# Performance work log

Hardware: AMD Instinct MI355X
Metric: run time of the kernel (lower is better)

## Reference

```python
import jax, jax.numpy as jnp
import numpy as np

N_NODES = 100000
N_EDGES = 1600000
D_IN = 256
D_HID = 128
N_CLASSES = 64
NEG_SLOPE = 0.2


def setup_inputs() -> dict:
    key = jax.random.key(0)
    ks = jax.random.split(key, 8)
    node_features = jax.random.normal(ks[0], (N_NODES, D_IN), dtype=jnp.float32)
    W = jax.random.normal(ks[1], (D_IN, D_HID), dtype=jnp.float32) * (1.0 / np.sqrt(D_IN))
    attn_l = jax.random.normal(ks[2], (D_HID,), dtype=jnp.float32) * (1.0 / np.sqrt(D_HID))
    attn_r = jax.random.normal(ks[3], (D_HID,), dtype=jnp.float32) * (1.0 / np.sqrt(D_HID))
    fc_W = jax.random.normal(ks[4], (D_HID, N_CLASSES), dtype=jnp.float32) * (1.0 / np.sqrt(D_HID))
    fc_b = jnp.zeros((N_CLASSES,), dtype=jnp.float32)
    src = jax.random.randint(ks[5], (N_EDGES,), 0, N_NODES, dtype=jnp.int32)
    dst = jax.random.randint(ks[6], (N_EDGES,), 0, N_NODES, dtype=jnp.int32)
    return dict(node_features=node_features, W=W, attn_l=attn_l, attn_r=attn_r,
                fc_W=fc_W, fc_b=fc_b, src=src, dst=dst)


def reference(node_features, W, attn_l, attn_r, fc_W, fc_b, src, dst):
    N = node_features.shape[0]
    # GATConv (single head): linear projection
    feat = node_features @ W                       # [N, H]
    el = feat @ attn_l                             # [N]
    er = feat @ attn_r                             # [N]
    e = jax.nn.leaky_relu(el[src] + er[dst], NEG_SLOPE)  # [E]
    # segment softmax over incoming edges of each destination node
    m = jax.ops.segment_max(e, dst, num_segments=N)      # [N]
    ex = jnp.exp(e - m[dst])                              # [E]
    denom = jax.ops.segment_sum(ex, dst, num_segments=N)  # [N]
    a = ex / denom[dst]                                   # [E]
    # attention-weighted neighbor aggregation (scatter-add)
    msg = a[:, None] * feat[src]                           # [E, H]
    h = jax.ops.segment_sum(msg, dst, num_segments=N)     # [N, H]
    # num_heads=1 -> h.mean(1) over heads is identity; final Linear
    return h @ fc_W + fc_b                                 # [N, C]
```

## Files before the change

### kernel.cpp

```cpp
#include <hip/hip_runtime.h>
#include <math.h>

#define NN 100000
#define NE 1600000
#define DIN 256
#define DHID 128
#define NCLS 64
#define NEG_SLOPE 0.2f

#define NBUCK 196
#define ECAP 10240
#define CHUNK 4096
#define NCHB ((NE + CHUNK - 1) / CHUNK)
#define PREPB 16

#define NGRP 16384
#define G1 ((NN + 127) / 128)

typedef __bf16 bf16_t;
typedef bf16_t bf16x8 __attribute__((ext_vector_type(8)));
typedef float f32x4 __attribute__((ext_vector_type(4)));
typedef ushort ushort8v __attribute__((ext_vector_type(8)));

__device__ __forceinline__ ushort f2bf(float f) {
    union { float f; unsigned u; } c; c.f = f;
    unsigned u = c.u;
    unsigned r = (u + 0x7FFFu + ((u >> 16) & 1u)) >> 16;
    return (ushort)r;
}
__device__ __forceinline__ float bf2f(ushort b) {
    return __uint_as_float(((unsigned)b) << 16);
}

__global__ __launch_bounds__(256) void k_prep(const float* __restrict__ W,
                                              const float* __restrict__ fcW,
                                              ushort* __restrict__ Wt,
                                              ushort* __restrict__ fcWt,
                                              int* __restrict__ gcur) {
    int t = blockIdx.x * 256 + threadIdx.x;
    if (blockIdx.x == 0) gcur[threadIdx.x] = 0;
    for (int i = t; i < DHID * DIN; i += PREPB * 256) {
        int n = i >> 8, k = i & 255;
        Wt[i] = f2bf(W[k * DHID + n]);
    }
    for (int i = t; i < NCLS * DHID; i += PREPB * 256) {
        int n = i >> 7, k = i & 127;
        fcWt[i] = f2bf(fcW[k * NCLS + n]);
    }
}

union SmemB {
    struct {
        int hist[NBUCK];
        int scn[256];
        int loff[NBUCK];
        int cur[NBUCK];
        int gb[NBUCK];
        unsigned ord[CHUNK];
        ushort obk[CHUNK];
    } b;
    struct {
        ushort Xs[2][8192];
        ushort Wl[2][8192];
        float Al[DHID];
        float Ar[DHID];
    } g;
};

#define ISSUE(XA, WA, KC) do { \
    int k0g_ = (KC) * 64; \
    _Pragma("unroll") \
    for (int i_ = 0; i_ < 4; i_++) { \
        int grow_ = row0 + srow[i_]; \
        if (grow_ < NN) { \
            const float4* p_ = (const float4*)(X + (size_t)grow_ * DIN + k0g_ + ske[i_]); \
            XA[i_][0] = p_[0]; XA[i_][1] = p_[1]; \
        } else { \
            XA[i_][0] = make_float4(0.f,0.f,0.f,0.f); \
            XA[i_][1] = make_float4(0.f,0.f,0.f,0.f); \
        } \
        WA[i_] = *(const uint4*)(Wt + (size_t)srow[i_] * DIN + k0g_ + ske[i_]); \
    } \
} while (0)

#define COMMIT(XA, WA, BUF) do { \
    _Pragma("unroll") \
    for (int i_ = 0; i_ < 4; i_++) { \
        int o_ = i_ * 4096 + t * 16; \
        ushort8v bb_; \
        bb_[0] = f2bf(XA[i_][0].x); bb_[1] = f2bf(XA[i_][0].y); \
        bb_[2] = f2bf(XA[i_][0].z); bb_[3] = f2bf(XA[i_][0].w); \
        bb_[4] = f2bf(XA[i_][1].x); bb_[5] = f2bf(XA[i_][1].y); \
        bb_[6] = f2bf(XA[i_][1].z); bb_[7] = f2bf(XA[i_][1].w); \
        *(ushort8v*)((char*)&sm.g.Xs[BUF][0] + o_) = bb_; \
        *(uint4*)((char*)&sm.g.Wl[BUF][0] + o_) = WA[i_]; \
    } \
} while (0)

#define COMPUTE(BUF) do { \
    const char* xb_ = (const char*)&sm.g.Xs[BUF][0]; \
    const char* wb_ = (const char*)&sm.g.Wl[BUF][0]; \
    _Pragma("unroll") \
    for (int k0_ = 0; k0_ < 2; k0_++) { \
        int kb_ = k0_ * 64 + kgrp; \
        bf16x8 a_[2], b_[8]; \
        _Pragma("unroll") \
        for (int r_ = 0; r_ < 2; r_++) { \
            int row_ = rbase + r_ * 16 + lcol; \
            a_[r_] = *(const bf16x8*)(xb_ + row_ * 128 + (kb_ ^ ((row_ & 7) << 4))); \
        } \
        _Pragma("unroll") \
        for (int cc_ = 0; cc_ < 8; cc_++) { \
            int n_ = cc_ * 16 + lcol; \
            b_[cc_] = *(const bf16x8*)(wb_ + n_ * 128 + (kb_ ^ ((n_ & 7) << 4))); \
        } \
        _Pragma("unroll") \
        for (int r_ = 0; r_ < 2; r_++) \
            _Pragma("unroll") \
            for (int cc_ = 0; cc_ < 8; cc_++) \
                acc[r_][cc_] = __builtin_amdgcn_mfma_f32_16x16x32_bf16(a_[r_], b_[cc_], acc[r_][cc_], 0, 0, 0); \
    } \
} while (0)

__global__ __launch_bounds__(256, 2) void fused_bin_gemm1(
        const int* __restrict__ src, const int* __restrict__ dst,
        int* __restrict__ gcur, unsigned* __restrict__ ebuf,
        const float* __restrict__ X, const ushort* __restrict__ Wt,
        const float* __restrict__ attn_l, const float* __restrict__ attn_r,
        ushort* __restrict__ featb, float* __restrict__ el, float* __restrict__ er) {
    __shared__ SmemB sm;
    const int t = threadIdx.x;

    if (blockIdx.x < NCHB) {
        const int base = blockIdx.x * CHUNK;
        int cnt = NE - base; if (cnt > CHUNK) cnt = CHUNK;

        for (int i = t; i < NBUCK; i += 256) sm.b.hist[i] = 0;
        __syncthreads();

        unsigned vals[16];
        int bks[16];
#pragma unroll
        for (int i = 0; i < 16; i++) {
            int idx = base + i * 256 + t;
            if (idx < NE) {
                int d = dst[idx], s = src[idx];
                int bb = d >> 9;
                bks[i] = bb;
                vals[i] = ((unsigned)(d & 511) << 17) | (unsigned)s;
                atomicAdd(&sm.b.hist[bb], 1);
            } else bks[i] = -1;
        }
        __syncthreads();

        int hv = (t < NBUCK) ? sm.b.hist[t] : 0;
        sm.b.scn[t] = hv;
        __syncthreads();
        for (int d = 1; d < 256; d <<= 1) {
            int a = (t >= d) ? sm.b.scn[t - d] : 0;
            __syncthreads();
            sm.b.scn[t] += a;
            __syncthreads();
        }
        if (t < NBUCK) { sm.b.loff[t] = sm.b.scn[t] - hv; sm.b.cur[t] = sm.b.scn[t] - hv; }
        __syncthreads();

#pragma unroll
        for (int i = 0; i < 16; i++) {
            if (bks[i] >= 0) {
                int slot = atomicAdd(&sm.b.cur[bks[i]], 1);
                sm.b.ord[slot] = vals[i];
                sm.b.obk[slot] = (ushort)bks[i];
            }
        }
        if (t < NBUCK && hv > 0) sm.b.gb[t] = t * ECAP + atomicAdd(&gcur[t], hv);
        __syncthreads();

        for (int s = t; s < cnt; s += 256) {
            int bb = sm.b.obk[s];
            ebuf[sm.b.gb[bb] + (s - sm.b.loff[bb])] = sm.b.ord[s];
        }
        return;
    }

    const int row0 = (blockIdx.x - NCHB) * 128;
    if (t < 128) { sm.g.Al[t] = attn_l[t]; sm.g.Ar[t] = attn_r[t]; }

    int srow[4], ske[4];
#pragma unroll
    for (int i = 0; i < 4; i++) {
        int o = i * 4096 + t * 16;
        int row = o >> 7;
        int bl = (o & 127) ^ ((row & 7) << 4);
        srow[i] = row;
        ske[i] = bl >> 1;
    }

    const int w = t >> 6, lane = t & 63;
    const int rbase = w * 32;
    const int lcol = lane & 15;
    const int kgrp = (lane >> 4) * 16;

    f32x4 acc[2][8];
#pragma unroll
    for (int r = 0; r < 2; r++)
#pragma unroll
        for (int c = 0; c < 8; c++) acc[r][c] = (f32x4){0.f, 0.f, 0.f, 0.f};

    float4 xA[4][2], xB[4][2];
    uint4  wA[4], wB[4];

    ISSUE(xA, wA, 0); COMMIT(xA, wA, 0);
    ISSUE(xB, wB, 1);
    __syncthreads();
    ISSUE(xA, wA, 2); COMPUTE(0); COMMIT(xB, wB, 1); __syncthreads();
    ISSUE(xB, wB, 3); COMPUTE(1); COMMIT(xA, wA, 0); __syncthreads();
    COMPUTE(0); COMMIT(xB, wB, 1); __syncthreads();
    COMPUTE(1);

    __syncthreads();
    ushort* Os = (ushort*)sm.g.Xs;
#pragma unroll
    for (int r = 0; r < 2; r++)
#pragma unroll
        for (int cc = 0; cc < 8; cc++)
#pragma unroll
            for (int i = 0; i < 4; i++) {
                int rloc = rbase + r * 16 + (lane >> 4) * 4 + i;
                int col = cc * 16 + lcol;
                Os[rloc * 128 + col] = f2bf(acc[r][cc][i]);
            }
    __syncthreads();

    {
        int row = t >> 1, half = t & 1;
        int grow = row0 + row;
        const ushort* orow = Os + row * 128 + half * 64;
        const float* alp = sm.g.Al + half * 64;
        const float* arp = sm.g.Ar + half * 64;
        float pl = 0.f, pr = 0.f;
        int rot = row & 7;
#pragma unroll
        for (int qq = 0; qq < 8; qq++) {
            int q = (qq + rot) & 7;
            ushort8v f8 = *(const ushort8v*)(orow + q * 8);
#pragma unroll
            for (int e = 0; e < 8; e++) {
                float fe = bf2f(f8[e]);
                pl += fe * alp[q * 8 + e];
                pr += fe * arp[q * 8 + e];
            }
        }
        pl += __shfl_down(pl, 1);
        pr += __shfl_down(pr, 1);
        if (!half && grow < NN) { el[grow] = pl; er[grow] = pr; }
    }

#pragma unroll
    for (int i = 0; i < 8; i++) {
        int u = i * 256 + t;
        int row = u >> 4;
        int grow = row0 + row;
        if (grow < NN)
            *(uint4*)(featb + (size_t)grow * 128 + (u & 15) * 8) =
                *(uint4*)((char*)Os + u * 16);
    }
}

__global__ __launch_bounds__(1024) void fused_csr(const unsigned* __restrict__ ebuf,
                                                  const int* __restrict__ gcur,
                                                  int* __restrict__ off_g,
                                                  int* __restrict__ deg_g,
                                                  int* __restrict__ ssrc,
                                                  int* __restrict__ nsplit) {
    __shared__ int sdeg[512];
    __shared__ int pr[256];
    __shared__ int lofs[512];
    __shared__ int scnt[512];
    __shared__ int sb[2];
    const int b = blockIdx.x, t = threadIdx.x;
    const int node0 = b << 9;
    const int ebase = b * ECAP;
    const int ecnt = gcur[b];

    if (t < 256) pr[t] = (t < NBUCK) ? gcur[t] : 0;
    __syncthreads();
    for (int d = 1; d < 256; d <<= 1) {
        int a = 0;
        if (t < 256 && t >= d) a = pr[t - d];
        __syncthreads();
        if (t < 256) pr[t] += a;
        __syncthreads();
    }
    if (t == 0) { sb[0] = pr[b] - ecnt; sb[1] = pr[NBUCK - 1]; }
    if (t < 512) sdeg[t] = 0;
    __syncthreads();

    for (int s = t; s < ecnt; s += 1024)
        atomicAdd(&sdeg[ebuf[ebase + s] >> 17], 1);
    __syncthreads();

    int d0 = 0, d1 = 0;
    if (t < 256) { d0 = sdeg[2 * t]; d1 = sdeg[2 * t + 1]; pr[t] = d0 + d1; }
    __syncthreads();
    for (int d = 1; d < 256; d <<= 1) {
        int a = 0;
        if (t < 256 && t >= d) a = pr[t - d];
        __syncthreads();
        if (t < 256) pr[t] += a;
        __syncthreads();
    }
    if (t < 256) {
        int ex = pr[t] - d0 - d1;
        lofs[2 * t] = ex;
        lofs[2 * t + 1] = ex + d0;
        scnt[2 * t] = 0; scnt[2 * t + 1] = 0;
        int n0 = node0 + 2 * t, n1 = n0 + 1;
        if (n0 < NN) { off_g[n0] = ebase + ex;      deg_g[n0] = d0; }
        if (n1 < NN) { off_g[n1] = ebase + ex + d0; deg_g[n1] = d1; }
    }
    __syncthreads();

    for (int s = t; s < ecnt; s += 1024) {
        unsigned v = ebuf[ebase + s];
        int dl = v >> 17;
        int c = atomicAdd(&scnt[dl], 1);
        ssrc[ebase + lofs[dl] + c] = (int)(v & 0x1FFFFu);
    }

    {
        long bpre_b = sb[0], total = sb[1];
        if (total > 0 && ecnt > 0) {
            long glo = (bpre_b * NGRP + total - 1) / total;
            long ghi = ((bpre_b + ecnt) * NGRP + total - 1) / total;
            if (ghi > NGRP) ghi = NGRP;
            for (long g = glo + t; g < ghi; g += 1024) {
                long target = g * total / NGRP;
                int lt = (int)(target - bpre_b);
                int lo = 0, hi = 512;
                while (lo < hi) {
                    int m = (lo + hi) >> 1;
                    if (lofs[m] < lt) lo = m + 1; else hi = m;
                }
                int node = node0 + lo;
                if (node > NN) node = NN;
                nsplit[g] = node;
            }
        }
        if (b == 0 && t == 0) nsplit[NGRP] = NN;
    }
}

__global__ __launch_bounds__(256) void aggregate(const int* __restrict__ off,
                                                 const int* __restrict__ deg,
                                                 const int* __restrict__ ssrc,
                                                 const float* __restrict__ el,
                                                 const float* __restrict__ er,
                                                 const ushort* __restrict__ featb,
                                                 ushort* __restrict__ hb,
                                                 const int* __restrict__ nsplit) {
    const int gid = blockIdx.x * 16 + (threadIdx.x >> 4);
    const int lc = threadIdx.x & 15;
    int n = nsplit[gid];
    const int nend = nsplit[gid + 1];
    const ushort* fb = featb + lc * 8;

    for (; n < nend; ++n) {
        const int e0 = off[n];
        const int dg = deg[n];
        const float erd = er[n];
        float acc[8];
#pragma unroll
        for (int q = 0; q < 8; q++) acc[q] = 0.f;
        float wsum = 0.f;

        int j = 0;
        for (; j + 4 <= dg; j += 4) {
            int s0 = ssrc[e0 + j + 0];
            int s1 = ssrc[e0 + j + 1];
            int s2 = ssrc[e0 + j + 2];
            int s3 = ssrc[e0 + j + 3];
            ushort8v f0 = *(const ushort8v*)(fb + (size_t)s0 * DHID);
            ushort8v f1 = *(const ushort8v*)(fb + (size_t)s1 * DHID);
            ushort8v f2 = *(const ushort8v*)(fb + (size_t)s2 * DHID);
            ushort8v f3 = *(const ushort8v*)(fb + (size_t)s3 * DHID);
            float x0 = el[s0] + erd, x1 = el[s1] + erd;
            float x2 = el[s2] + erd, x3 = el[s3] + erd;
            x0 = x0 > 0.f ? x0 : NEG_SLOPE * x0;
            x1 = x1 > 0.f ? x1 : NEG_SLOPE * x1;
            x2 = x2 > 0.f ? x2 : NEG_SLOPE * x2;
            x3 = x3 > 0.f ? x3 : NEG_SLOPE * x3;
            float w0 = __expf(x0), w1 = __expf(x1);
            float w2 = __expf(x2), w3 = __expf(x3);
            wsum += (w0 + w1) + (w2 + w3);
#pragma unroll
            for (int q = 0; q < 8; q++)
                acc[q] += (w0 * bf2f(f0[q]) + w1 * bf2f(f1[q])) +
                          (w2 * bf2f(f2[q]) + w3 * bf2f(f3[q]));
        }
        for (; j < dg; ++j) {
            int s0 = ssrc[e0 + j];
            ushort8v f0 = *(const ushort8v*)(fb + (size_t)s0 * DHID);
            float x0 = el[s0] + erd;
            x0 = x0 > 0.f ? x0 : NEG_SLOPE * x0;
            float w0 = __expf(x0);
            wsum += w0;
#pragma unroll
            for (int q = 0; q < 8; q++) acc[q] += w0 * bf2f(f0[q]);
        }

        float inv = (dg > 0) ? 1.0f / wsum : 0.f;
        ushort8v o8;
#pragma unroll
        for (int q = 0; q < 8; q++) o8[q] = f2bf(acc[q] * inv);
        *(ushort8v*)(hb + (size_t)n * DHID + lc * 8) = o8;
    }
}

__global__ __launch_bounds__(256, 3) void gemm2(const ushort* __restrict__ hb,
                                                const ushort* __restrict__ fcWt,
                                                const float* __restrict__ fcb,
                                                float* __restrict__ out) {
    __shared__ ushort Hs[128 * 128];
    __shared__ ushort Fs[64 * 128];
    const int t = threadIdx.x;
    const int row0 = blockIdx.x * 128;

    {
#pragma unroll
        for (int i = 0; i < 8; i++) {
            int u = i * 256 + t;
            int row = u >> 4;
            int grow = row0 + row;
            uint4 v = make_uint4(0, 0, 0, 0);
            if (grow < NN) v = *(const uint4*)(hb + (size_t)grow * 128 + (u & 15) * 8);
            int byte_off = row * 256 + (((u & 15) * 16) ^ ((row & 7) << 4));
            *(uint4*)((char*)Hs + byte_off) = v;
        }
#pragma unroll
        for (int i = 0; i < 4; i++) {
            int u = i * 256 + t;
            int n = u >> 4;
            int byte_off = n * 256 + (((u & 15) * 16) ^ ((n & 7) << 4));
            *(uint4*)((char*)Fs + byte_off) = ((const uint4*)fcWt)[u];
        }
    }

    const int w = t >> 6, lane = t & 63;
    const int rbase = w * 32;
    const int lcol = lane & 15;
    const int kgrp = (lane >> 4) * 16;

    f32x4 acc[2][4];
#pragma unroll
    for (int c = 0; c < 4; c++) {
        float bias = fcb[c * 16 + lcol];
#pragma unroll
        for (int r = 0; r < 2; r++)
#pragma unroll
            for (int i = 0; i < 4; i++) acc[r][c][i] = bias;
    }
    __syncthreads();

#pragma unroll
    for (int k0 = 0; k0 < 4; k0++) {
        int kbyte = k0 * 64 + kgrp;
        bf16x8 a[2], b[4];
#pragma unroll
        for (int r = 0; r < 2; r++) {
            int row = rbase + r * 16 + lcol;
            a[r] = *(bf16x8*)((char*)Hs + row * 256 + (kbyte ^ ((row & 7) << 4)));
        }
#pragma unroll
        for (int c = 0; c < 4; c++) {
            int n = c * 16 + lcol;
            b[c] = *(bf16x8*)((char*)Fs + n * 256 + (kbyte ^ ((n & 7) << 4)));
        }
#pragma unroll
        for (int r = 0; r < 2; r++)
#pragma unroll
            for (int c = 0; c < 4; c++)
                acc[r][c] = __builtin_amdgcn_mfma_f32_16x16x32_bf16(a[r], b[c], acc[r][c], 0, 0, 0);
    }

#pragma unroll
    for (int r = 0; r < 2; r++)
#pragma unroll
        for (int i = 0; i < 4; i++) {
            int row = rbase + r * 16 + (lane >> 4) * 4 + i;
            int grow = row0 + row;
            if (grow < NN) {
                float* op = out + (size_t)grow * 64 + lcol;
#pragma unroll
                for (int c = 0; c < 4; c++) op[c * 16] = acc[r][c][i];
            }
        }
}

extern "C" void kernel_launch(void* const* d_in, const int* in_sizes, int n_in,
                              void* d_out, int out_size, void* d_ws, size_t ws_size,
                              hipStream_t stream) {
    const float* X      = (const float*)d_in[0];
    const float* W      = (const float*)d_in[1];
    const float* attn_l = (const float*)d_in[2];
    const float* attn_r = (const float*)d_in[3];
    const float* fcW    = (const float*)d_in[4];
    const float* fcb    = (const float*)d_in[5];
    const int*   src    = (const int*)d_in[6];
    const int*   dst    = (const int*)d_in[7];
    float* out = (float*)d_out;

    char* ws = (char*)d_ws;
    ushort* featb = (ushort*)ws;            ws += (size_t)NN * DHID * 2;
    ushort* hb    = (ushort*)ws;            ws += (size_t)NN * DHID * 2;
    ushort* Wt    = (ushort*)ws;            ws += (size_t)DHID * DIN * 2;
    ushort* fcWt  = (ushort*)ws;            ws += (size_t)NCLS * DHID * 2;
    float* el     = (float*)ws;             ws += (size_t)NN * 4;
    float* er     = (float*)ws;             ws += (size_t)NN * 4;
    int*   deg    = (int*)ws;               ws += (size_t)NN * 4;
    int*   off    = (int*)ws;               ws += (size_t)NN * 4;
    int*   ssrc   = (int*)ws;               ws += (size_t)NBUCK * ECAP * 4;
    unsigned* ebuf = (unsigned*)ws;         ws += (size_t)NBUCK * ECAP * 4;
    int*   gcur   = (int*)ws;               ws += (size_t)256 * 4;
    int*   nsplit = (int*)ws;               ws += (size_t)(NGRP + 1) * 4;

    k_prep<<<PREPB, 256, 0, stream>>>(W, fcW, Wt, fcWt, gcur);
    fused_bin_gemm1<<<NCHB + G1, 256, 0, stream>>>(src, dst, gcur, ebuf,
                                                   X, Wt, attn_l, attn_r, featb, el, er);
    fused_csr<<<NBUCK, 1024, 0, stream>>>(ebuf, gcur, off, deg, ssrc, nsplit);
    aggregate<<<NGRP / 16, 256, 0, stream>>>(off, deg, ssrc, el, er, featb, hb, nsplit);
    gemm2<<<(NN + 127) / 128, 256, 0, stream>>>(hb, fcWt, fcb, out);
}
```

Before: 160.8 us.

## Shrink GEMM1 K-chunk to 32 and raise occupancy to four blocks

Restructures the first-layer projection GEMM to stage 32-wide K slices instead of 64-wide ones, using a loop of eight double-buffered steps with a 64-byte row swizzle. This halves the per-thread prefetch registers and the LDS tile buffers. It also raises launch bounds from 2 to 4 blocks per SM, aiming to hide global-load latency through more resident waves. The trade-off is twice as many block barriers and less MFMA work between them, plus a new swizzle pattern that may bring LDS bank conflicts.

```diff
diff --git a/kernel.cpp b/kernel.cpp
--- a/kernel.cpp
+++ b/kernel.cpp
@@ -60,69 +60,14 @@
         ushort obk[CHUNK];
     } b;
     struct {
-        ushort Xs[2][8192];
-        ushort Wl[2][8192];
+        ushort Xs[2][4096];
+        ushort Wl[2][4096];
         float Al[DHID];
         float Ar[DHID];
     } g;
 };
 
-#define ISSUE(XA, WA, KC) do { \
-    int k0g_ = (KC) * 64; \
-    _Pragma("unroll") \
-    for (int i_ = 0; i_ < 4; i_++) { \
-        int grow_ = row0 + srow[i_]; \
-        if (grow_ < NN) { \
-            const float4* p_ = (const float4*)(X + (size_t)grow_ * DIN + k0g_ + ske[i_]); \
-            XA[i_][0] = p_[0]; XA[i_][1] = p_[1]; \
-        } else { \
-            XA[i_][0] = make_float4(0.f,0.f,0.f,0.f); \
-            XA[i_][1] = make_float4(0.f,0.f,0.f,0.f); \
-        } \
-        WA[i_] = *(const uint4*)(Wt + (size_t)srow[i_] * DIN + k0g_ + ske[i_]); \
-    } \
-} while (0)
-
-#define COMMIT(XA, WA, BUF) do { \
-    _Pragma("unroll") \
-    for (int i_ = 0; i_ < 4; i_++) { \
-        int o_ = i_ * 4096 + t * 16; \
-        ushort8v bb_; \
-        bb_[0] = f2bf(XA[i_][0].x); bb_[1] = f2bf(XA[i_][0].y); \
-        bb_[2] = f2bf(XA[i_][0].z); bb_[3] = f2bf(XA[i_][0].w); \
-        bb_[4] = f2bf(XA[i_][1].x); bb_[5] = f2bf(XA[i_][1].y); \
-        bb_[6] = f2bf(XA[i_][1].z); bb_[7] = f2bf(XA[i_][1].w); \
-        *(ushort8v*)((char*)&sm.g.Xs[BUF][0] + o_) = bb_; \
-        *(uint4*)((char*)&sm.g.Wl[BUF][0] + o_) = WA[i_]; \
-    } \
-} while (0)
-
-#define COMPUTE(BUF) do { \
-    const char* xb_ = (const char*)&sm.g.Xs[BUF][0]; \
-    const char* wb_ = (const char*)&sm.g.Wl[BUF][0]; \
-    _Pragma("unroll") \
-    for (int k0_ = 0; k0_ < 2; k0_++) { \
-        int kb_ = k0_ * 64 + kgrp; \
-        bf16x8 a_[2], b_[8]; \
-        _Pragma("unroll") \
-        for (int r_ = 0; r_ < 2; r_++) { \
-            int row_ = rbase + r_ * 16 + lcol; \
-            a_[r_] = *(const bf16x8*)(xb_ + row_ * 128 + (kb_ ^ ((row_ & 7) << 4))); \
-        } \
-        _Pragma("unroll") \
-        for (int cc_ = 0; cc_ < 8; cc_++) { \
-            int n_ = cc_ * 16 + lcol; \
-            b_[cc_] = *(const bf16x8*)(wb_ + n_ * 128 + (kb_ ^ ((n_ & 7) << 4))); \
-        } \
-        _Pragma("unroll") \
-        for (int r_ = 0; r_ < 2; r_++) \
-            _Pragma("unroll") \
-            for (int cc_ = 0; cc_ < 8; cc_++) \
-                acc[r_][cc_] = __builtin_amdgcn_mfma_f32_16x16x32_bf16(a_[r_], b_[cc_], acc[r_][cc_], 0, 0, 0); \
-    } \
-} while (0)
-
-__global__ __launch_bounds__(256, 2) void fused_bin_gemm1(
+__global__ __launch_bounds__(256, 4) void fused_bin_gemm1(
         const int* __restrict__ src, const int* __restrict__ dst,
         int* __restrict__ gcur, unsigned* __restrict__ ebuf,
         const float* __restrict__ X, const ushort* __restrict__ Wt,
@@ -186,20 +131,23 @@
     const int row0 = (blockIdx.x - NCHB) * 128;
     if (t < 128) { sm.g.Al[t] = attn_l[t]; sm.g.Ar[t] = attn_r[t]; }
 
-    int srow[4], ske[4];
-#pragma unroll
-    for (int i = 0; i < 4; i++) {
-        int o = i * 4096 + t * 16;
-        int row = o >> 7;
-        int bl = (o & 127) ^ ((row & 7) << 4);
+    int srow[2], sc16[2], sbyte[2];
+    bool sval[2];
+#pragma unroll
+    for (int i = 0; i < 2; i++) {
+        int u = i * 256 + t;
+        int row = u >> 2;
+        int c16 = u & 3;
         srow[i] = row;
-        ske[i] = bl >> 1;
+        sc16[i] = c16;
+        sbyte[i] = row * 64 + ((c16 * 16) ^ ((row & 3) << 4));
+        sval[i] = (row0 + row) < NN;
     }
 
     const int w = t >> 6, lane = t & 63;
     const int rbase = w * 32;
     const int lcol = lane & 15;
-    const int kgrp = (lane >> 4) * 16;
+    const int kgrpB = (lane >> 4) * 16;
 
     f32x4 acc[2][8];
 #pragma unroll
@@ -207,18 +155,70 @@
 #pragma unroll
         for (int c = 0; c < 8; c++) acc[r][c] = (f32x4){0.f, 0.f, 0.f, 0.f};
 
-    float4 xA[4][2], xB[4][2];
-    uint4  wA[4], wB[4];
-
-    ISSUE(xA, wA, 0); COMMIT(xA, wA, 0);
-    ISSUE(xB, wB, 1);
-    __syncthreads();
-    ISSUE(xA, wA, 2); COMPUTE(0); COMMIT(xB, wB, 1); __syncthreads();
-    ISSUE(xB, wB, 3); COMPUTE(1); COMMIT(xA, wA, 0); __syncthreads();
-    COMPUTE(0); COMMIT(xB, wB, 1); __syncthreads();
-    COMPUTE(1);
-
-    __syncthreads();
+    float4 xf[2][2];
+    uint4  wreg[2];
+
+#define G1_ISSUE(KC) do { \
+    _Pragma("unroll") \
+    for (int i_ = 0; i_ < 2; i_++) { \
+        if (sval[i_]) { \
+            const float4* p_ = (const float4*)(X + (size_t)(row0 + srow[i_]) * DIN + (KC) * 32 + sc16[i_] * 8); \
+            xf[i_][0] = p_[0]; xf[i_][1] = p_[1]; \
+        } else { \
+            xf[i_][0] = make_float4(0.f,0.f,0.f,0.f); \
+            xf[i_][1] = make_float4(0.f,0.f,0.f,0.f); \
+        } \
+        wreg[i_] = *(const uint4*)(Wt + (size_t)srow[i_] * DIN + (KC) * 32 + sc16[i_] * 8); \
+    } \
+} while (0)
+
+#define G1_COMMIT(BUF) do { \
+    _Pragma("unroll") \
+    for (int i_ = 0; i_ < 2; i_++) { \
+        ushort8v bb_; \
+        bb_[0] = f2bf(xf[i_][0].x); bb_[1] = f2bf(xf[i_][0].y); \
+        bb_[2] = f2bf(xf[i_][0].z); bb_[3] = f2bf(xf[i_][0].w); \
+        bb_[4] = f2bf(xf[i_][1].x); bb_[5] = f2bf(xf[i_][1].y); \
+        bb_[6] = f2bf(xf[i_][1].z); bb_[7] = f2bf(xf[i_][1].w); \
+        *(ushort8v*)((char*)&sm.g.Xs[BUF][0] + sbyte[i_]) = bb_; \
+        *(uint4*)((char*)&sm.g.Wl[BUF][0] + sbyte[i_]) = wreg[i_]; \
+    } \
+} while (0)
+
+#define G1_COMPUTE(BUF) do { \
+    const char* xb_ = (const char*)&sm.g.Xs[BUF][0]; \
+    const char* wb_ = (const char*)&sm.g.Wl[BUF][0]; \
+    bf16x8 a_[2], b_[8]; \
+    _Pragma("unroll") \
+    for (int r_ = 0; r_ < 2; r_++) { \
+        int row_ = rbase + r_ * 16 + lcol; \
+        a_[r_] = *(const bf16x8*)(xb_ + row_ * 64 + (kgrpB ^ ((row_ & 3) << 4))); \
+    } \
+    _Pragma("unroll") \
+    for (int cc_ = 0; cc_ < 8; cc_++) { \
+        int n_ = cc_ * 16 + lcol; \
+        b_[cc_] = *(const bf16x8*)(wb_ + n_ * 64 + (kgrpB ^ ((n_ & 3) << 4))); \
+    } \
+    _Pragma("unroll") \
+    for (int r_ = 0; r_ < 2; r_++) \
+        _Pragma("unroll") \
+        for (int cc_ = 0; cc_ < 8; cc_++) \
+            acc[r_][cc_] = __builtin_amdgcn_mfma_f32_16x16x32_bf16(a_[r_], b_[cc_], acc[r_][cc_], 0, 0, 0); \
+} while (0)
+
+    G1_ISSUE(0);
+    G1_COMMIT(0);
+    __syncthreads();
+#pragma unroll
+    for (int c = 0; c < 8; c++) {
+        if (c < 7) G1_ISSUE(c + 1);
+        if (c & 1) { G1_COMPUTE(1); } else { G1_COMPUTE(0); }
+        if (c < 7) {
+            if ((c + 1) & 1) { G1_COMMIT(1); } else { G1_COMMIT(0); }
+        }
+        __syncthreads();
+    }
+
     ushort* Os = (ushort*)sm.g.Xs;
 #pragma unroll
     for (int r = 0; r < 2; r++)
```

Measured after the change: 156.9 us. 1.02x faster.
